# Performance work log

Hardware: AMD Instinct MI355X
Metric: run time of the kernel (lower is better)

The kernel has to match this reference:

```python
import jax, jax.numpy as jnp
import numpy as np
from jax import lax

DIM = 1024
HID = 2048          # dim * hidden_mult(2)
E = 8               # num_experts
K = 2               # top_k
B, T = 2, 512


def setup_inputs() -> dict:
    key = jax.random.key(0)
    ks = jax.random.split(key, 5)
    scale = 1.0 / np.sqrt(DIM)
    x = jax.random.normal(ks[0], (B, T, DIM), dtype=jnp.float32)
    router_w = jax.random.normal(ks[1], (E, DIM), dtype=jnp.float32) * scale   # Linear(dim, E) weight (out,in)
    w_gate = jax.random.normal(ks[2], (E, HID, DIM), dtype=jnp.float32) * scale
    w_up = jax.random.normal(ks[3], (E, HID, DIM), dtype=jnp.float32) * scale
    w_down = jax.random.normal(ks[4], (E, DIM, HID), dtype=jnp.float32) * (1.0 / np.sqrt(HID))
    return {"x": x, "router_w": router_w, "w_gate": w_gate, "w_up": w_up, "w_down": w_down}


def reference(x, router_w, w_gate, w_up, w_down):
    Bb, Tt, D = x.shape
    N = Bb * Tt
    xf = x.reshape(N, D)
    # router + top-k gating (weights renormalized over selected experts)
    logits = xf @ router_w.T                                   # (N, E)
    routing = jax.nn.softmax(logits, axis=-1)
    top_w, top_i = lax.top_k(routing, K)                       # (N, K)
    top_w = top_w / jnp.sum(top_w, axis=-1, keepdims=True)
    # combine weights: per-token weight for each expert (0 if not selected).
    # Multiplying by 0 reproduces the mask-gather-scatter loop exactly.
    combine = jnp.zeros((N, E), dtype=x.dtype)
    combine = combine.at[jnp.arange(N)[:, None], top_i].add(top_w)  # (N, E)
    # SwiGLU experts, batched over the (small, fixed) expert axis
    g = jnp.einsum('nd,ehd->neh', xf, w_gate)                  # (N, E, H)
    u = jnp.einsum('nd,ehd->neh', xf, w_up)
    h = jax.nn.silu(g) * u
    y = jnp.einsum('neh,edh->ned', h, w_down)                  # (N, E, D)
    out = jnp.einsum('ned,ne->nd', y, combine)
    return out.reshape(Bb, Tt, D)
```

## Files before the change

### kernel.cpp

```cpp
#include <hip/hip_runtime.h>
#include <hip/hip_bf16.h>
#include <math.h>

#define DIM 1024
#define HID 2048
#define NEXP 8
#define NTOK 1024
#define TOPK 2

typedef __attribute__((ext_vector_type(4))) float f32x4;
typedef __attribute__((ext_vector_type(8))) short bf16x8;
typedef __attribute__((ext_vector_type(4))) short bf16x4;

__device__ inline short bf1(float f) {
    union { __hip_bfloat16 b; short s; } u; u.b = __float2bfloat16(f); return u.s;
}
__device__ inline bf16x4 cvt4(f32x4 v) {
    bf16x4 r;
#pragma unroll
    for (int i = 0; i < 4; ++i) r[i] = bf1(v[i]);
    return r;
}
__device__ inline bf16x8 cat8(bf16x4 lo, bf16x4 hi) {
    bf16x8 r;
#pragma unroll
    for (int i = 0; i < 4; ++i) { r[i] = lo[i]; r[i + 4] = hi[i]; }
    return r;
}

__global__ __launch_bounds__(64) void router_kernel(
    const float* __restrict__ x, const float* __restrict__ rw,
    __hip_bfloat16* __restrict__ xb,
    int* __restrict__ counts, int* __restrict__ slot_list, float* __restrict__ w_list)
{
    int t = blockIdx.x;
    int lane = threadIdx.x;
    const float* xr = x + (size_t)t * DIM;
    f32x4 xv[4];
#pragma unroll
    for (int qq = 0; qq < 4; ++qq) xv[qq] = *(const f32x4*)(xr + qq * 256 + lane * 4);
#pragma unroll
    for (int qq = 0; qq < 4; ++qq)
        *(bf16x4*)(xb + (size_t)t * DIM + qq * 256 + lane * 4) = cvt4(xv[qq]);

    float acc[NEXP];
#pragma unroll
    for (int e = 0; e < NEXP; ++e) {
        const float* rwe = rw + e * DIM;
        f32x4 s4 = (f32x4)(0.f);
#pragma unroll
        for (int qq = 0; qq < 4; ++qq) {
            f32x4 wv = *(const f32x4*)(rwe + qq * 256 + lane * 4);
            s4 += xv[qq] * wv;
        }
        acc[e] = s4[0] + s4[1] + s4[2] + s4[3];
    }
#pragma unroll
    for (int off = 32; off > 0; off >>= 1) {
#pragma unroll
        for (int e = 0; e < NEXP; ++e) acc[e] += __shfl_down(acc[e], off, 64);
    }
    if (lane == 0) {
        int i1 = 0;
#pragma unroll
        for (int e = 1; e < NEXP; ++e) if (acc[e] > acc[i1]) i1 = e;
        int i2 = -1;
#pragma unroll
        for (int e = 0; e < NEXP; ++e) {
            if (e == i1) continue;
            if (i2 < 0 || acc[e] > acc[i2]) i2 = e;
        }
        float w1 = 1.f / (1.f + expf(acc[i2] - acc[i1]));
        float w2 = 1.f - w1;
        int p1 = atomicAdd(&counts[i1], 1);
        slot_list[i1 * NTOK + p1] = t * 2 + 0;
        w_list[i1 * NTOK + p1] = w1;
        int p2 = atomicAdd(&counts[i2], 1);
        slot_list[i2 * NTOK + p2] = t * 2 + 1;
        w_list[i2 * NTOK + p2] = w2;
    }
}

__global__ __launch_bounds__(256) void gateup_mfma(
    const __hip_bfloat16* __restrict__ xb, const float* __restrict__ wg,
    const float* __restrict__ wu, const int* __restrict__ counts,
    const int* __restrict__ slot_list, const float* __restrict__ w_list,
    const __hip_bfloat16* __restrict__ zrow, __hip_bfloat16* __restrict__ h_buf)
{
    __shared__ short Xs[2][64 * 64];
    __shared__ short Gs[2][64 * 64];
    __shared__ short Us[2][64 * 64];

    int bid = blockIdx.x;
    int pl = bid & 7, sfold = bid >> 3;
    int z = sfold & 3, ph = sfold >> 2;
    int p = (ph << 3) | pl;
    int e = p >> 5;
    int hbase = (p & 31) * 64;

    int n_e = counts[e];
    if (n_e == 0) return;
    const int* sl = slot_list + e * NTOK;
    const float* wl = w_list + e * NTOK;
    const float* WG = wg + (size_t)e * HID * DIM;
    const float* WU = wu + (size_t)e * HID * DIM;

    int tid = threadIdx.x;
    int lane = tid & 63;
    int wn = tid >> 6;
    int fr = lane & 15, fq = lane >> 4;

    int r2 = tid >> 3;
    int j = tid & 7;
    int sw = (j ^ (r2 & 7)) * 8;

    const float* g0 = WG + (size_t)(hbase + r2) * DIM + j * 8;
    const float* g1 = g0 + (size_t)32 * DIM;
    const float* u0 = WU + (size_t)(hbase + r2) * DIM + j * 8;
    const float* u1 = u0 + (size_t)32 * DIM;

    for (int m0 = z * 64; m0 < n_e; m0 += 256) {
        int rows = n_e - m0; if (rows > 64) rows = 64;
        const __hip_bfloat16* x0 = (r2 < rows) ? xb + (size_t)(sl[m0 + r2] >> 1) * DIM + j * 8 : zrow + j * 8;
        const __hip_bfloat16* x1 = (r2 + 32 < rows) ? xb + (size_t)(sl[m0 + r2 + 32] >> 1) * DIM + j * 8 : zrow + j * 8;

        f32x4 accg[4], accu[4];
#pragma unroll
        for (int ms = 0; ms < 4; ++ms) { accg[ms] = (f32x4)(0.f); accu[ms] = (f32x4)(0.f); }

        bf16x8 sx[2][2];
        f32x4 sg[2][4], su[2][4];
#pragma unroll
        for (int st = 0; st < 2; ++st) {
            int ko = st * 64;
            sx[st][0] = *(const bf16x8*)(x0 + ko);
            sx[st][1] = *(const bf16x8*)(x1 + ko);
            sg[st][0] = *(const f32x4*)(g0 + ko);
            sg[st][1] = *(const f32x4*)(g0 + ko + 4);
            sg[st][2] = *(const f32x4*)(g1 + ko);
            sg[st][3] = *(const f32x4*)(g1 + ko + 4);
            su[st][0] = *(const f32x4*)(u0 + ko);
            su[st][1] = *(const f32x4*)(u0 + ko + 4);
            su[st][2] = *(const f32x4*)(u1 + ko);
            su[st][3] = *(const f32x4*)(u1 + ko + 4);
        }

#pragma unroll 1
        for (int tt = 0; tt < DIM / 64; tt += 2) {
#pragma unroll
            for (int half = 0; half < 2; ++half) {
                *(bf16x8*)&Xs[half][r2 * 64 + sw] = sx[half][0];
                *(bf16x8*)&Xs[half][(r2 + 32) * 64 + sw] = sx[half][1];
                *(bf16x8*)&Gs[half][r2 * 64 + sw] = cat8(cvt4(sg[half][0]), cvt4(sg[half][1]));
                *(bf16x8*)&Gs[half][(r2 + 32) * 64 + sw] = cat8(cvt4(sg[half][2]), cvt4(sg[half][3]));
                *(bf16x8*)&Us[half][r2 * 64 + sw] = cat8(cvt4(su[half][0]), cvt4(su[half][1]));
                *(bf16x8*)&Us[half][(r2 + 32) * 64 + sw] = cat8(cvt4(su[half][2]), cvt4(su[half][3]));
                int k2 = (tt + half + 2) * 64;
                if (k2 < DIM) {
                    sx[half][0] = *(const bf16x8*)(x0 + k2);
                    sx[half][1] = *(const bf16x8*)(x1 + k2);
                    sg[half][0] = *(const f32x4*)(g0 + k2);
                    sg[half][1] = *(const f32x4*)(g0 + k2 + 4);
                    sg[half][2] = *(const f32x4*)(g1 + k2);
                    sg[half][3] = *(const f32x4*)(g1 + k2 + 4);
                    su[half][0] = *(const f32x4*)(u0 + k2);
                    su[half][1] = *(const f32x4*)(u0 + k2 + 4);
                    su[half][2] = *(const f32x4*)(u1 + k2);
                    su[half][3] = *(const f32x4*)(u1 + k2 + 4);
                }
                __syncthreads();
#pragma unroll
                for (int kk = 0; kk < 2; ++kk) {
                    int co = ((kk * 4 + fq) ^ (fr & 7)) * 8;
                    bf16x8 bg = *(const bf16x8*)&Gs[half][(wn * 16 + fr) * 64 + co];
                    bf16x8 bu = *(const bf16x8*)&Us[half][(wn * 16 + fr) * 64 + co];
#pragma unroll
                    for (int ms = 0; ms < 4; ++ms) {
                        bf16x8 a = *(const bf16x8*)&Xs[half][(ms * 16 + fr) * 64 + co];
                        accg[ms] = __builtin_amdgcn_mfma_f32_16x16x32_bf16(a, bg, accg[ms], 0, 0, 0);
                        accu[ms] = __builtin_amdgcn_mfma_f32_16x16x32_bf16(a, bu, accu[ms], 0, 0, 0);
                    }
                }
            }
        }

#pragma unroll
        for (int ms = 0; ms < 4; ++ms) {
#pragma unroll
            for (int reg = 0; reg < 4; ++reg) {
                int r = ms * 16 + fq * 4 + reg;
                if (r < rows) {
                    int slot = sl[m0 + r];
                    float w = wl[m0 + r];
                    float g = accg[ms][reg], u = accu[ms][reg];
                    float h = w * (g / (1.f + expf(-g))) * u;
                    h_buf[(size_t)slot * HID + hbase + wn * 16 + fr] = __float2bfloat16(h);
                }
            }
        }
    }
}

__global__ __launch_bounds__(256) void down_mfma(
    const __hip_bfloat16* __restrict__ h_buf, const float* __restrict__ wd,
    const int* __restrict__ counts, const int* __restrict__ slot_list,
    const __hip_bfloat16* __restrict__ zrow, float* __restrict__ ybuf)
{
    __shared__ short Hs[2][64 * 64];
    __shared__ short Ws[2][64 * 64];

    int bid = blockIdx.x;
    int pl = bid & 7, sfold = bid >> 3;
    int z = sfold & 3, qh = sfold >> 2;
    int q = (qh << 3) | pl;
    int e = q >> 4;
    int dbase = (q & 15) * 64;

    int n_e = counts[e];
    if (n_e == 0) return;
    const int* sl = slot_list + e * NTOK;
    const float* WD = wd + (size_t)e * DIM * HID;

    int tid = threadIdx.x;
    int lane = tid & 63;
    int wn = tid >> 6;
    int fr = lane & 15, fq = lane >> 4;

    int r2 = tid >> 3;
    int j = tid & 7;
    int sw = (j ^ (r2 & 7)) * 8;

    const float* w0 = WD + (size_t)(dbase + r2) * HID + j * 8;
    const float* w1 = w0 + (size_t)32 * HID;

    for (int m0 = z * 64; m0 < n_e; m0 += 256) {
        int rows = n_e - m0; if (rows > 64) rows = 64;
        const __hip_bfloat16* h0 = (r2 < rows) ? h_buf + (size_t)sl[m0 + r2] * HID + j * 8 : zrow + j * 8;
        const __hip_bfloat16* h1 = (r2 + 32 < rows) ? h_buf + (size_t)sl[m0 + r2 + 32] * HID + j * 8 : zrow + j * 8;

        f32x4 acc[4];
#pragma unroll
        for (int ms = 0; ms < 4; ++ms) acc[ms] = (f32x4)(0.f);

        bf16x8 sh[2][2];
        f32x4 sd[2][4];
#pragma unroll
        for (int st = 0; st < 2; ++st) {
            int ko = st * 64;
            sh[st][0] = *(const bf16x8*)(h0 + ko);
            sh[st][1] = *(const bf16x8*)(h1 + ko);
            sd[st][0] = *(const f32x4*)(w0 + ko);
            sd[st][1] = *(const f32x4*)(w0 + ko + 4);
            sd[st][2] = *(const f32x4*)(w1 + ko);
            sd[st][3] = *(const f32x4*)(w1 + ko + 4);
        }

#pragma unroll 1
        for (int tt = 0; tt < HID / 64; tt += 2) {
#pragma unroll
            for (int half = 0; half < 2; ++half) {
                *(bf16x8*)&Hs[half][r2 * 64 + sw] = sh[half][0];
                *(bf16x8*)&Hs[half][(r2 + 32) * 64 + sw] = sh[half][1];
                *(bf16x8*)&Ws[half][r2 * 64 + sw] = cat8(cvt4(sd[half][0]), cvt4(sd[half][1]));
                *(bf16x8*)&Ws[half][(r2 + 32) * 64 + sw] = cat8(cvt4(sd[half][2]), cvt4(sd[half][3]));
                int k2 = (tt + half + 2) * 64;
                if (k2 < HID) {
                    sh[half][0] = *(const bf16x8*)(h0 + k2);
                    sh[half][1] = *(const bf16x8*)(h1 + k2);
                    sd[half][0] = *(const f32x4*)(w0 + k2);
                    sd[half][1] = *(const f32x4*)(w0 + k2 + 4);
                    sd[half][2] = *(const f32x4*)(w1 + k2);
                    sd[half][3] = *(const f32x4*)(w1 + k2 + 4);
                }
                __syncthreads();
#pragma unroll
                for (int kk = 0; kk < 2; ++kk) {
                    int co = ((kk * 4 + fq) ^ (fr & 7)) * 8;
                    bf16x8 b = *(const bf16x8*)&Ws[half][(wn * 16 + fr) * 64 + co];
#pragma unroll
                    for (int ms = 0; ms < 4; ++ms) {
                        bf16x8 a = *(const bf16x8*)&Hs[half][(ms * 16 + fr) * 64 + co];
                        acc[ms] = __builtin_amdgcn_mfma_f32_16x16x32_bf16(a, b, acc[ms], 0, 0, 0);
                    }
                }
            }
        }

#pragma unroll
        for (int ms = 0; ms < 4; ++ms) {
#pragma unroll
            for (int reg = 0; reg < 4; ++reg) {
                int r = ms * 16 + fq * 4 + reg;
                if (r < rows) {
                    int slot = sl[m0 + r];
                    ybuf[(size_t)slot * DIM + dbase + wn * 16 + fr] = acc[ms][reg];
                }
            }
        }
    }
}

__global__ __launch_bounds__(256) void combine_kernel(const float* __restrict__ ybuf, float* __restrict__ out)
{
    int i = blockIdx.x * 256 + threadIdx.x;
    int t = i >> 8;
    int c = i & 255;
    const float4* ya = (const float4*)(ybuf + (size_t)(2 * t) * DIM) + c;
    const float4* yb = (const float4*)(ybuf + (size_t)(2 * t + 1) * DIM) + c;
    float4 a = *ya, b = *yb, r;
    r.x = a.x + b.x; r.y = a.y + b.y; r.z = a.z + b.z; r.w = a.w + b.w;
    ((float4*)(out + (size_t)t * DIM))[c] = r;
}

extern "C" void kernel_launch(void* const* d_in, const int* in_sizes, int n_in,
                              void* d_out, int out_size, void* d_ws, size_t ws_size,
                              hipStream_t stream) {
    const float* x  = (const float*)d_in[0];
    const float* rw = (const float*)d_in[1];
    const float* wg = (const float*)d_in[2];
    const float* wu = (const float*)d_in[3];
    const float* wd = (const float*)d_in[4];
    float* out = (float*)d_out;

    char* ws = (char*)d_ws;
    int* counts            = (int*)ws;
    int* slot_list         = (int*)(ws + 256);
    float* w_list          = (float*)(ws + 256 + NEXP * NTOK * 4);
    __hip_bfloat16* xb     = (__hip_bfloat16*)(ws + 256 + 2 * NEXP * NTOK * 4);
    __hip_bfloat16* h_buf  = (__hip_bfloat16*)((char*)xb + (size_t)NTOK * DIM * 2);
    float* ybuf            = (float*)((char*)h_buf + (size_t)NTOK * TOPK * HID * 2);
    __hip_bfloat16* zrow   = (__hip_bfloat16*)((char*)ybuf + (size_t)NTOK * TOPK * DIM * 4);

    hipMemsetAsync(counts, 0, NEXP * sizeof(int), stream);
    hipMemsetAsync(zrow, 0, HID * sizeof(__hip_bfloat16), stream);
    router_kernel<<<NTOK, 64, 0, stream>>>(x, rw, xb, counts, slot_list, w_list);
    gateup_mfma<<<1024, 256, 0, stream>>>(xb, wg, wu, counts, slot_list, w_list, zrow, h_buf);
    down_mfma<<<512, 256, 0, stream>>>(h_buf, wd, counts, slot_list, zrow, ybuf);
    combine_kernel<<<NTOK * DIM / 4 / 256, 256, 0, stream>>>(ybuf, out);
}
```

Baseline: 152.8 us.

## Pre-convert gate/up weights to bf16 in separate kernels before gate-up GEMM

Adds a grid-stride conversion kernel that turns the fp32 gate and up weights into bf16 copies in workspace on every call. The gate-up GEMM then loads bf16 directly, with no in-loop conversion and half the register staging. It also adds a trailing __syncthreads after each compute half in both GEMMs to guard the double-buffered shared tiles. The conversion reads and writes all weights each call, which adds memory traffic that likely outweighs the savings, and the extra barriers add sync cost.

```diff
diff --git a/kernel.cpp b/kernel.cpp
--- a/kernel.cpp
+++ b/kernel.cpp
@@ -26,6 +26,16 @@
 #pragma unroll
     for (int i = 0; i < 4; ++i) { r[i] = lo[i]; r[i + 4] = hi[i]; }
     return r;
+}
+
+__global__ __launch_bounds__(256) void wcvt_kernel(const float* __restrict__ in,
+                                                   __hip_bfloat16* __restrict__ outb, int n4)
+{
+    int stride = gridDim.x * 256;
+    for (int i = blockIdx.x * 256 + threadIdx.x; i < n4; i += stride) {
+        f32x4 v = *(const f32x4*)(in + (size_t)i * 4);
+        *(bf16x4*)(outb + (size_t)i * 4) = cvt4(v);
+    }
 }
 
 __global__ __launch_bounds__(64) void router_kernel(
@@ -82,8 +92,8 @@
 }
 
 __global__ __launch_bounds__(256) void gateup_mfma(
-    const __hip_bfloat16* __restrict__ xb, const float* __restrict__ wg,
-    const float* __restrict__ wu, const int* __restrict__ counts,
+    const __hip_bfloat16* __restrict__ xb, const __hip_bfloat16* __restrict__ wgb,
+    const __hip_bfloat16* __restrict__ wub, const int* __restrict__ counts,
     const int* __restrict__ slot_list, const float* __restrict__ w_list,
     const __hip_bfloat16* __restrict__ zrow, __hip_bfloat16* __restrict__ h_buf)
 {
@@ -102,8 +112,6 @@
     if (n_e == 0) return;
     const int* sl = slot_list + e * NTOK;
     const float* wl = w_list + e * NTOK;
-    const float* WG = wg + (size_t)e * HID * DIM;
-    const float* WU = wu + (size_t)e * HID * DIM;
 
     int tid = threadIdx.x;
     int lane = tid & 63;
@@ -114,10 +122,10 @@
     int j = tid & 7;
     int sw = (j ^ (r2 & 7)) * 8;
 
-    const float* g0 = WG + (size_t)(hbase + r2) * DIM + j * 8;
-    const float* g1 = g0 + (size_t)32 * DIM;
-    const float* u0 = WU + (size_t)(hbase + r2) * DIM + j * 8;
-    const float* u1 = u0 + (size_t)32 * DIM;
+    const __hip_bfloat16* g0 = wgb + (size_t)e * HID * DIM + (size_t)(hbase + r2) * DIM + j * 8;
+    const __hip_bfloat16* g1 = g0 + (size_t)32 * DIM;
+    const __hip_bfloat16* u0 = wub + (size_t)e * HID * DIM + (size_t)(hbase + r2) * DIM + j * 8;
+    const __hip_bfloat16* u1 = u0 + (size_t)32 * DIM;
 
     for (int m0 = z * 64; m0 < n_e; m0 += 256) {
         int rows = n_e - m0; if (rows > 64) rows = 64;
@@ -128,21 +136,16 @@
 #pragma unroll
         for (int ms = 0; ms < 4; ++ms) { accg[ms] = (f32x4)(0.f); accu[ms] = (f32x4)(0.f); }
 
-        bf16x8 sx[2][2];
-        f32x4 sg[2][4], su[2][4];
+        bf16x8 sx[2][2], sg[2][2], su[2][2];
 #pragma unroll
         for (int st = 0; st < 2; ++st) {
             int ko = st * 64;
             sx[st][0] = *(const bf16x8*)(x0 + ko);
             sx[st][1] = *(const bf16x8*)(x1 + ko);
-            sg[st][0] = *(const f32x4*)(g0 + ko);
-            sg[st][1] = *(const f32x4*)(g0 + ko + 4);
-            sg[st][2] = *(const f32x4*)(g1 + ko);
-            sg[st][3] = *(const f32x4*)(g1 + ko + 4);
-            su[st][0] = *(const f32x4*)(u0 + ko);
-            su[st][1] = *(const f32x4*)(u0 + ko + 4);
-            su[st][2] = *(const f32x4*)(u1 + ko);
-            su[st][3] = *(const f32x4*)(u1 + ko + 4);
+            sg[st][0] = *(const bf16x8*)(g0 + ko);
+            sg[st][1] = *(const bf16x8*)(g1 + ko);
+            su[st][0] = *(const bf16x8*)(u0 + ko);
+            su[st][1] = *(const bf16x8*)(u1 + ko);
         }
 
 #pragma unroll 1
@@ -151,22 +154,18 @@
             for (int half = 0; half < 2; ++half) {
                 *(bf16x8*)&Xs[half][r2 * 64 + sw] = sx[half][0];
                 *(bf16x8*)&Xs[half][(r2 + 32) * 64 + sw] = sx[half][1];
-                *(bf16x8*)&Gs[half][r2 * 64 + sw] = cat8(cvt4(sg[half][0]), cvt4(sg[half][1]));
-                *(bf16x8*)&Gs[half][(r2 + 32) * 64 + sw] = cat8(cvt4(sg[half][2]), cvt4(sg[half][3]));
-                *(bf16x8*)&Us[half][r2 * 64 + sw] = cat8(cvt4(su[half][0]), cvt4(su[half][1]));
-                *(bf16x8*)&Us[half][(r2 + 32) * 64 + sw] = cat8(cvt4(su[half][2]), cvt4(su[half][3]));
+                *(bf16x8*)&Gs[half][r2 * 64 + sw] = sg[half][0];
+                *(bf16x8*)&Gs[half][(r2 + 32) * 64 + sw] = sg[half][1];
+                *(bf16x8*)&Us[half][r2 * 64 + sw] = su[half][0];
+                *(bf16x8*)&Us[half][(r2 + 32) * 64 + sw] = su[half][1];
                 int k2 = (tt + half + 2) * 64;
                 if (k2 < DIM) {
                     sx[half][0] = *(const bf16x8*)(x0 + k2);
                     sx[half][1] = *(const bf16x8*)(x1 + k2);
-                    sg[half][0] = *(const f32x4*)(g0 + k2);
-                    sg[half][1] = *(const f32x4*)(g0 + k2 + 4);
-                    sg[half][2] = *(const f32x4*)(g1 + k2);
-                    sg[half][3] = *(const f32x4*)(g1 + k2 + 4);
-                    su[half][0] = *(const f32x4*)(u0 + k2);
-                    su[half][1] = *(const f32x4*)(u0 + k2 + 4);
-                    su[half][2] = *(const f32x4*)(u1 + k2);
-                    su[half][3] = *(const f32x4*)(u1 + k2 + 4);
+                    sg[half][0] = *(const bf16x8*)(g0 + k2);
+                    sg[half][1] = *(const bf16x8*)(g1 + k2);
+                    su[half][0] = *(const bf16x8*)(u0 + k2);
+                    su[half][1] = *(const bf16x8*)(u1 + k2);
                 }
                 __syncthreads();
 #pragma unroll
@@ -181,6 +180,7 @@
                         accu[ms] = __builtin_amdgcn_mfma_f32_16x16x32_bf16(a, bu, accu[ms], 0, 0, 0);
                     }
                 }
+                __syncthreads();
             }
         }
 
@@ -283,6 +283,7 @@
                         acc[ms] = __builtin_amdgcn_mfma_f32_16x16x32_bf16(a, b, acc[ms], 0, 0, 0);
                     }
                 }
+                __syncthreads();
             }
         }
 
@@ -330,11 +331,17 @@
     __hip_bfloat16* h_buf  = (__hip_bfloat16*)((char*)xb + (size_t)NTOK * DIM * 2);
     float* ybuf            = (float*)((char*)h_buf + (size_t)NTOK * TOPK * HID * 2);
     __hip_bfloat16* zrow   = (__hip_bfloat16*)((char*)ybuf + (size_t)NTOK * TOPK * DIM * 4);
+    __hip_bfloat16* wgb    = (__hip_bfloat16*)((char*)zrow + 8192);
+    __hip_bfloat16* wub    = (__hip_bfloat16*)((char*)wgb + (size_t)NEXP * HID * DIM * 2);
+
+    const int W4 = NEXP * HID * DIM / 4;
 
     hipMemsetAsync(counts, 0, NEXP * sizeof(int), stream);
     hipMemsetAsync(zrow, 0, HID * sizeof(__hip_bfloat16), stream);
+    wcvt_kernel<<<2048, 256, 0, stream>>>(wg, wgb, W4);
+    wcvt_kernel<<<2048, 256, 0, stream>>>(wu, wub, W4);
     router_kernel<<<NTOK, 64, 0, stream>>>(x, rw, xb, counts, slot_list, w_list);
-    gateup_mfma<<<1024, 256, 0, stream>>>(xb, wg, wu, counts, slot_list, w_list, zrow, h_buf);
+    gateup_mfma<<<1024, 256, 0, stream>>>(xb, wgb, wub, counts, slot_list, w_list, zrow, h_buf);
     down_mfma<<<512, 256, 0, stream>>>(h_buf, wd, counts, slot_list, zrow, ybuf);
     combine_kernel<<<NTOK * DIM / 4 / 256, 256, 0, stream>>>(ybuf, out);
 }
```

Result: slower. 174.8 us (+14.4%).
